# Kernel tuning notes

Measured on AMD Instinct MI355X. Metric: run time of the kernel, lower is better.

## Reference

```python
import jax, jax.numpy as jnp
import numpy as np
from jax import lax

B, C, H, W, K = 32, 128, 56, 56, 5
CR = C // 4          # reduced channels in weight-gen MLP
CE = 4 * C           # expanded channels
EPS = 1e-6


def setup_inputs() -> dict:
    key = jax.random.key(0)
    ks = jax.random.split(key, 8)
    s = lambda fan: 1.0 / np.sqrt(fan)
    return {
        "x": jax.random.normal(ks[0], (B, C, H, W), jnp.float32),
        "w_fc1": jax.random.normal(ks[1], (CR, C), jnp.float32) * s(C),
        "ln1_w": jnp.ones((CR,), jnp.float32),
        "ln1_b": jnp.zeros((CR,), jnp.float32),
        "w_fc2": jax.random.normal(ks[2], (C * K * K, CR), jnp.float32) * s(CR),
        "ln2_w": jnp.ones((C,), jnp.float32),
        "ln2_b": jnp.zeros((C,), jnp.float32),
        "w_expand": jax.random.normal(ks[3], (CE, C), jnp.float32) * s(C),
        "w_shrink": jax.random.normal(ks[4], (C, CE), jnp.float32) * s(CE),
        "grn_gamma": jax.random.normal(ks[5], (CE,), jnp.float32) * 0.1,
        "grn_beta": jax.random.normal(ks[6], (CE,), jnp.float32) * 0.1,
    }


def _ln(v, w, b, axis):
    u = v.mean(axis, keepdims=True)
    s2 = jnp.square(v - u).mean(axis, keepdims=True)
    return (v - u) * lax.rsqrt(s2 + EPS) * w + b


def reference(x, w_fc1, ln1_w, ln1_b, w_fc2, ln2_w, ln2_b, w_expand, w_shrink,
              grn_gamma, grn_beta):
    b, c, h, w = x.shape
    # ---- dynamic weight generation: pool -> fc1 -> LN -> fc2 ----
    pooled = x.mean((2, 3))                                  # [B, C]
    hdn = pooled @ w_fc1.T                                   # [B, CR]
    hdn = _ln(hdn, ln1_w, ln1_b, axis=-1)                    # channels_first LN over CR
    dyn = hdn @ w_fc2.T                                      # [B, C*K*K]
    dyn_w = dyn.reshape(b * c, 1, K, K)                      # per-sample depthwise kernels
    # ---- per-sample dynamic depthwise conv (groups = B*C) ----
    pad = K // 2
    out = lax.conv_general_dilated(
        x.reshape(1, b * c, h, w), dyn_w,
        window_strides=(1, 1), padding=[(pad, pad), (pad, pad)],
        dimension_numbers=("NCHW", "OIHW", "NCHW"),
        feature_group_count=b * c,
    ).reshape(b, c, h, w)
    # ---- LN (channels_first) over channel dim ----
    u = out.mean(1, keepdims=True)
    s2 = jnp.square(out - u).mean(1, keepdims=True)
    out = (out - u) * lax.rsqrt(s2 + EPS)
    out = ln2_w[None, :, None, None] * out + ln2_b[None, :, None, None]
    # ---- expand 1x1 -> GELU -> GRN -> shrink 1x1 ----
    out = jnp.einsum("bchw,oc->bohw", out, w_expand)         # [B, 4C, H, W]
    out = jax.nn.gelu(out, approximate=False)
    gx = jnp.sqrt(jnp.sum(jnp.square(out), axis=(2, 3), keepdims=True))  # [B,4C,1,1]
    nx = gx / (gx.mean(1, keepdims=True) + EPS)
    g = grn_gamma[None, :, None, None]
    bt = grn_beta[None, :, None, None]
    out = g * (out * nx) + bt + out
    out = jnp.einsum("bohw,co->bchw", out, w_shrink)         # [B, C, H, W]
    return out + x
```

## Files before the change

kernel.cpp:

```cpp
#include <hip/hip_runtime.h>
#include <hip/hip_bf16.h>

#define B_   32
#define C_   128
#define H_   56
#define W_   56
#define HW_  (H_*W_)
#define BHW_ (B_*HW_)
#define K5_  5
#define KK_  25
#define CR_  32
#define CE_  512
#define EPS_ 1e-6f

typedef __hip_bfloat16 bf16;
typedef __attribute__((ext_vector_type(8))) short short8;
typedef __attribute__((ext_vector_type(4))) float f32x4;


__device__ __forceinline__ float wave_reduce_sum(float v) {
#pragma unroll
  for (int off = 32; off > 0; off >>= 1) v += __shfl_down(v, off, 64);
  return v;
}
__device__ __forceinline__ float bf2f(unsigned short u) {
  return __uint_as_float(((unsigned)u) << 16);
}
__device__ __forceinline__ unsigned short f2bf_bits(float f) {
  bf16 h = __float2bfloat16(f);
  unsigned short u;
  __builtin_memcpy(&u, &h, 2);
  return u;
}
__device__ __forceinline__ float fast_gelu(float v) {
  float t = __expf(-1.702f * v);
  return v * __builtin_amdgcn_rcpf(1.0f + t);
}

__global__ __launch_bounds__(256) void prep_kernel(const float* __restrict__ we,
                                                   const float* __restrict__ ws,
                                                   bf16* __restrict__ weB,
                                                   bf16* __restrict__ wsB,
                                                   float* __restrict__ gx2) {
  int i = blockIdx.x * 256 + threadIdx.x;
  if (i < CE_ * C_)          weB[i] = __float2bfloat16(we[i]);
  else if (i < 2 * CE_ * C_) wsB[i - CE_ * C_] = __float2bfloat16(ws[i - CE_ * C_]);
  else                       gx2[i - 2 * CE_ * C_] = 0.f;
}

__global__ __launch_bounds__(256) void pool_kernel(const float* __restrict__ x,
                                                   float* __restrict__ pooled) {
  int bc = blockIdx.x;
  const float4* xp4 = reinterpret_cast<const float4*>(x + (size_t)bc * HW_);
  float s = 0.f;
  for (int i = threadIdx.x; i < 784; i += 256) {
    float4 v = xp4[i];
    s += (v.x + v.y) + (v.z + v.w);
  }
  s = wave_reduce_sum(s);
  __shared__ float red[4];
  int lane = threadIdx.x & 63, wid = threadIdx.x >> 6;
  if (lane == 0) red[wid] = s;
  __syncthreads();
  if (threadIdx.x == 0) pooled[bc] = (red[0] + red[1] + red[2] + red[3]) * (1.0f / HW_);
}

__global__ __launch_bounds__(256) void fc_kernel(const float* __restrict__ pooled,
                                                 const float* __restrict__ w_fc1,
                                                 const float* __restrict__ ln1_w,
                                                 const float* __restrict__ ln1_b,
                                                 const float* __restrict__ w_fc2,
                                                 float* __restrict__ dyn) {
  int b = blockIdx.x;
  int tid = threadIdx.x;
  __shared__ float sp[C_];
  __shared__ float sh[CR_];
  __shared__ float shn[CR_];
  __shared__ float stats[2];
  if (tid < C_) sp[tid] = pooled[b * C_ + tid];
  __syncthreads();
  if (tid < CR_) {
    float acc = 0.f;
    const float* wr = w_fc1 + tid * C_;
#pragma unroll 4
    for (int c = 0; c < C_; ++c) acc += sp[c] * wr[c];
    sh[tid] = acc;
  }
  __syncthreads();
  if (tid == 0) {
    float u = 0.f;
    for (int j = 0; j < CR_; ++j) u += sh[j];
    u *= (1.0f / CR_);
    float v = 0.f;
    for (int j = 0; j < CR_; ++j) { float d = sh[j] - u; v += d * d; }
    v *= (1.0f / CR_);
    stats[0] = u;
    stats[1] = rsqrtf(v + EPS_);
  }
  __syncthreads();
  if (tid < CR_) shn[tid] = (sh[tid] - stats[0]) * stats[1] * ln1_w[tid] + ln1_b[tid];
  __syncthreads();
  for (int i = tid; i < C_ * KK_; i += 256) {
    const float* wr = w_fc2 + i * CR_;
    float acc = 0.f;
#pragma unroll
    for (int j = 0; j < CR_; ++j) acc += shn[j] * wr[j];
    dyn[b * (C_ * KK_) + i] = acc;
  }
}

__global__ __launch_bounds__(256) void conv_kernel(const float* __restrict__ x,
                                                   const float* __restrict__ dyn,
                                                   bf16* __restrict__ z) {
  int bc = blockIdx.x;
  int b = bc >> 7;
  int c = bc & 127;
  int tid = threadIdx.x;
  __shared__ float xs[(H_ + 4) * 64];
  __shared__ float wks[KK_];
  {
    int r = tid >> 6;
    int rr = (r < 2) ? r : (56 + r);
    xs[rr * 64 + (tid & 63)] = 0.f;
  }
  if (tid < 224) {
    int r = tid >> 2, q = tid & 3;
    int col = (q < 2) ? q : (56 + q);
    xs[(r + 2) * 64 + col] = 0.f;
  }
  if (tid < KK_) wks[tid] = dyn[b * (C_ * KK_) + c * KK_ + tid];
  const float4* xp4 = reinterpret_cast<const float4*>(x + (size_t)bc * HW_);
  for (int i = tid; i < 784; i += 256) {
    float4 v = xp4[i];
    int h = i / 14, w4 = (i % 14) * 4;
    float* dst = &xs[(h + 2) * 64 + 2 + w4];
    dst[0] = v.x; dst[1] = v.y; dst[2] = v.z; dst[3] = v.w;
  }
  __syncthreads();
  float wr[KK_];
#pragma unroll
  for (int j = 0; j < KK_; ++j) wr[j] = wks[j];
  for (int g = tid; g < 784; g += 256) {
    int h = g / 14;
    int w4 = (g % 14) * 4;
    float a0 = 0.f, a1 = 0.f, a2 = 0.f, a3 = 0.f;
#pragma unroll
    for (int dh = 0; dh < K5_; ++dh) {
      const float* row = &xs[(h + dh) * 64 + w4];
      float4 va = *reinterpret_cast<const float4*>(row);
      float4 vb = *reinterpret_cast<const float4*>(row + 4);
      float v0 = va.x, v1 = va.y, v2 = va.z, v3 = va.w;
      float v4 = vb.x, v5 = vb.y, v6 = vb.z, v7 = vb.w;
      float u0 = wr[dh * 5 + 0], u1 = wr[dh * 5 + 1], u2 = wr[dh * 5 + 2];
      float u3 = wr[dh * 5 + 3], u4 = wr[dh * 5 + 4];
      a0 += v0 * u0 + v1 * u1 + v2 * u2 + v3 * u3 + v4 * u4;
      a1 += v1 * u0 + v2 * u1 + v3 * u2 + v4 * u3 + v5 * u4;
      a2 += v2 * u0 + v3 * u1 + v4 * u2 + v5 * u3 + v6 * u4;
      a3 += v3 * u0 + v4 * u1 + v5 * u2 + v6 * u3 + v7 * u4;
    }
    size_t base = (size_t)bc * HW_ + h * W_ + w4;
    ushort4 pk = make_ushort4(f2bf_bits(a0), f2bf_bits(a1), f2bf_bits(a2), f2bf_bits(a3));
    *reinterpret_cast<ushort4*>(reinterpret_cast<unsigned short*>(z) + base) = pk;
  }
}

__global__ __launch_bounds__(256) void ln_kernel(const bf16* __restrict__ z,
                                                 const float* __restrict__ ln2_w,
                                                 const float* __restrict__ ln2_b,
                                                 bf16* __restrict__ yT) {
  int hw0 = blockIdx.x * 64;
  int b = blockIdx.y;
  int tid = threadIdx.x;
  int wq = tid & 63;
  int cq = tid >> 6;
  __shared__ unsigned short zt[C_][64];
  __shared__ unsigned short yt[64][136];
  __shared__ float redS[4][64];
  __shared__ float redQ[4][64];
  __shared__ float meanArr[64];
  __shared__ float invArr[64];
  float s = 0.f, q = 0.f;
  const unsigned short* zp = reinterpret_cast<const unsigned short*>(z);
#pragma unroll 4
  for (int k = 0; k < 32; ++k) {
    int c = cq * 32 + k;
    unsigned short u = zp[((size_t)(b * C_ + c)) * HW_ + hw0 + wq];
    float v = bf2f(u);
    s += v;
    q += v * v;
    zt[c][wq] = u;
  }
  redS[cq][wq] = s;
  redQ[cq][wq] = q;
  __syncthreads();
  if (cq == 0) {
    float ss = redS[0][wq] + redS[1][wq] + redS[2][wq] + redS[3][wq];
    float qq = redQ[0][wq] + redQ[1][wq] + redQ[2][wq] + redQ[3][wq];
    float m = ss * (1.0f / C_);
    float var = qq * (1.0f / C_) - m * m;
    meanArr[wq] = m;
    invArr[wq] = rsqrtf(fmaxf(var, 0.f) + EPS_);
  }
  __syncthreads();
  float m = meanArr[wq], iv = invArr[wq];
#pragma unroll
  for (int g = 0; g < 4; ++g) {
    unsigned short pk[8];
#pragma unroll
    for (int i = 0; i < 8; ++i) {
      int c = cq * 32 + g * 8 + i;
      float v = bf2f(zt[c][wq]);
      pk[i] = f2bf_bits((v - m) * iv * ln2_w[c] + ln2_b[c]);
    }
    int4 t;
    __builtin_memcpy(&t, pk, 16);
    *reinterpret_cast<int4*>(&yt[wq][cq * 32 + g * 8]) = t;
  }
  __syncthreads();
  unsigned short* yp = reinterpret_cast<unsigned short*>(yT);
#pragma unroll
  for (int i = 0; i < 4; ++i) {
    int t = tid + 256 * i;
    int row = t >> 4, ch = t & 15;
    int4 v = *reinterpret_cast<const int4*>(&yt[row][ch * 8]);
    *reinterpret_cast<int4*>(yp + ((size_t)(b * HW_ + hw0 + row)) * C_ + ch * 8) = v;
  }
}

__global__ __launch_bounds__(256, 4) void expand_mfma(const bf16* __restrict__ yT,
                                                      const bf16* __restrict__ weB,
                                                      bf16* __restrict__ eT,
                                                      float* __restrict__ gx2) {
  int o0 = blockIdx.x * 128;
  int j0 = blockIdx.y * 128;
  int tid = threadIdx.x;
  int lane = tid & 63, wid = tid >> 6;
  int wm = wid >> 1, wn = wid & 1;
  int quad = lane >> 4, l15 = lane & 15;
  __shared__ __align__(16) char smem[128 * 136 * 2];
  short (*As)[40] = reinterpret_cast<short(*)[40]>(&smem[0]);
  short (*Bs)[40] = reinterpret_cast<short(*)[40]>(&smem[10240]);
  f32x4 acc[4][4] = {};
  const short* yTs = reinterpret_cast<const short*>(yT);
  const short* weS = reinterpret_cast<const short*>(weB);
  for (int k0 = 0; k0 < C_; k0 += 32) {
#pragma unroll
    for (int t = tid; t < 512; t += 256) {
      int r = t >> 2, ch = t & 3;
      int4 va = *reinterpret_cast<const int4*>(yTs + (size_t)(j0 + r) * C_ + k0 + ch * 8);
      *reinterpret_cast<int4*>(&As[r][ch * 8]) = va;
      int4 vb = *reinterpret_cast<const int4*>(weS + (size_t)(o0 + r) * C_ + k0 + ch * 8);
      *reinterpret_cast<int4*>(&Bs[r][ch * 8]) = vb;
    }
    __syncthreads();
    short8 a[4], bfr[4];
#pragma unroll
    for (int mf = 0; mf < 4; ++mf)
      a[mf] = *reinterpret_cast<const short8*>(&As[wm * 64 + mf * 16 + l15][quad * 8]);
#pragma unroll
    for (int nf = 0; nf < 4; ++nf)
      bfr[nf] = *reinterpret_cast<const short8*>(&Bs[wn * 64 + nf * 16 + l15][quad * 8]);
#pragma unroll
    for (int mf = 0; mf < 4; ++mf)
#pragma unroll
      for (int nf = 0; nf < 4; ++nf)
        acc[mf][nf] = __builtin_amdgcn_mfma_f32_16x16x32_bf16(a[mf], bfr[nf], acc[mf][nf], 0, 0, 0);
    __syncthreads();
  }
  short (*Es)[136] = reinterpret_cast<short(*)[136]>(&smem[0]);
#pragma unroll
  for (int mf = 0; mf < 4; ++mf) {
    int jm = j0 + wm * 64 + mf * 16;
    int bb = jm / HW_;
    int jrow = wm * 64 + mf * 16 + quad * 4;
#pragma unroll
    for (int nf = 0; nf < 4; ++nf) {
      int oc = wn * 64 + nf * 16 + l15;
      float g2 = 0.f;
#pragma unroll
      for (int r = 0; r < 4; ++r) {
        float ge = fast_gelu(acc[mf][nf][r]);
        g2 += ge * ge;
        Es[jrow + r][oc] = (short)f2bf_bits(ge);
      }
      g2 += __shfl_xor(g2, 16, 64);
      g2 += __shfl_xor(g2, 32, 64);
      if (quad == 0) atomicAdd(&gx2[bb * CE_ + o0 + oc], g2);
    }
  }
  __syncthreads();
  unsigned short* eP = reinterpret_cast<unsigned short*>(eT);
#pragma unroll
  for (int i = 0; i < 8; ++i) {
    int t = tid + 256 * i;
    int row = t >> 4, ch = t & 15;
    int4 v = *reinterpret_cast<const int4*>(&Es[row][ch * 8]);
    *reinterpret_cast<int4*>(eP + (size_t)(j0 + row) * CE_ + o0 + ch * 8) = v;
  }
}

__global__ __launch_bounds__(512) void grn_scale_kernel(const float* __restrict__ gx2,
                                                        const float* __restrict__ gamma,
                                                        float* __restrict__ scale) {
  int b = blockIdx.x;
  int o = threadIdx.x;
  float gx = sqrtf(gx2[b * CE_ + o]);
  float s = wave_reduce_sum(gx);
  __shared__ float red[8];
  __shared__ float meansh;
  int lane = o & 63, wid = o >> 6;
  if (lane == 0) red[wid] = s;
  __syncthreads();
  if (o == 0) {
    float t = 0.f;
    for (int i = 0; i < 8; ++i) t += red[i];
    meansh = t * (1.0f / CE_);
  }
  __syncthreads();
  scale[b * CE_ + o] = 1.0f + gamma[o] * (gx / (meansh + EPS_));
}

__global__ __launch_bounds__(256) void sb_kernel(const float* __restrict__ w_shrink,
                                                 const float* __restrict__ beta,
                                                 float* __restrict__ sb) {
  int c = blockIdx.x;
  const float* wp = w_shrink + (size_t)c * CE_;
  float acc = 0.f;
  for (int o = threadIdx.x; o < CE_; o += 256) acc += wp[o] * beta[o];
  acc = wave_reduce_sum(acc);
  __shared__ float red[4];
  int lane = threadIdx.x & 63, wid = threadIdx.x >> 6;
  if (lane == 0) red[wid] = acc;
  __syncthreads();
  if (threadIdx.x == 0) sb[c] = red[0] + red[1] + red[2] + red[3];
}

__global__ __launch_bounds__(256, 4) void shrink_mfma(const bf16* __restrict__ eT,
                                                      const bf16* __restrict__ wsB,
                                                      const float* __restrict__ scale,
                                                      const float* __restrict__ sb,
                                                      const float* __restrict__ x,
                                                      float* __restrict__ out) {
  int hw0 = blockIdx.x * 128;
  int b = blockIdx.y;
  int tid = threadIdx.x;
  int lane = tid & 63, wid = tid >> 6;
  int wm = wid >> 1, wn = wid & 1;
  int quad = lane >> 4, l15 = lane & 15;
  __shared__ __align__(16) char smem[36864];
  short (*As)[72] = reinterpret_cast<short(*)[72]>(&smem[0]);
  short (*Bs)[72] = reinterpret_cast<short(*)[72]>(&smem[18432]);
  const short* eS  = reinterpret_cast<const short*>(eT) + (size_t)b * HW_ * CE_;
  const short* wsS = reinterpret_cast<const short*>(wsB);
  const float* scp = scale + b * CE_;
  f32x4 acc[4][4] = {};
#pragma unroll 1
  for (int kc = 0; kc < 8; ++kc) {
    int k0 = kc * 64;
#pragma unroll
    for (int i = 0; i < 4; ++i) {
      int t = tid + 256 * i;
      int row = t >> 3, ch = t & 7;
      int hwc = hw0 + row; if (hwc >= HW_) hwc = HW_ - 1;
      *reinterpret_cast<int4*>(&As[row][ch * 8]) =
          *reinterpret_cast<const int4*>(eS + (size_t)hwc * CE_ + k0 + ch * 8);
      int4 wv = *reinterpret_cast<const int4*>(wsS + (size_t)row * CE_ + k0 + ch * 8);
      float4 s0 = *reinterpret_cast<const float4*>(scp + k0 + ch * 8);
      float4 s1 = *reinterpret_cast<const float4*>(scp + k0 + ch * 8 + 4);
      unsigned short wu[8];
      __builtin_memcpy(wu, &wv, 16);
      unsigned short ru[8];
      ru[0] = f2bf_bits(bf2f(wu[0]) * s0.x);
      ru[1] = f2bf_bits(bf2f(wu[1]) * s0.y);
      ru[2] = f2bf_bits(bf2f(wu[2]) * s0.z);
      ru[3] = f2bf_bits(bf2f(wu[3]) * s0.w);
      ru[4] = f2bf_bits(bf2f(wu[4]) * s1.x);
      ru[5] = f2bf_bits(bf2f(wu[5]) * s1.y);
      ru[6] = f2bf_bits(bf2f(wu[6]) * s1.z);
      ru[7] = f2bf_bits(bf2f(wu[7]) * s1.w);
      int4 rv;
      __builtin_memcpy(&rv, ru, 16);
      *reinterpret_cast<int4*>(&Bs[row][ch * 8]) = rv;
    }
    __syncthreads();
#pragma unroll
    for (int ks = 0; ks < 2; ++ks) {
      short8 a[4], bfr[4];
#pragma unroll
      for (int mf = 0; mf < 4; ++mf)
        a[mf] = *reinterpret_cast<const short8*>(&As[wm * 64 + mf * 16 + l15][ks * 32 + quad * 8]);
#pragma unroll
      for (int nf = 0; nf < 4; ++nf)
        bfr[nf] = *reinterpret_cast<const short8*>(&Bs[wn * 64 + nf * 16 + l15][ks * 32 + quad * 8]);
#pragma unroll
      for (int mf = 0; mf < 4; ++mf)
#pragma unroll
        for (int nf = 0; nf < 4; ++nf)
          acc[mf][nf] = __builtin_amdgcn_mfma_f32_16x16x32_bf16(a[mf], bfr[nf], acc[mf][nf], 0, 0, 0);
    }
    __syncthreads();
  }
  float (*Ef)[132] = reinterpret_cast<float(*)[132]>(&smem[0]);
#pragma unroll 1
  for (int phase = 0; phase < 2; ++phase) {
    if (wn == phase) {
#pragma unroll
      for (int mf = 0; mf < 4; ++mf) {
        int hwr = wm * 64 + mf * 16 + quad * 4;
#pragma unroll
        for (int nf = 0; nf < 4; ++nf)
          *reinterpret_cast<f32x4*>(&Ef[nf * 16 + l15][hwr]) = acc[mf][nf];
      }
    }
    __syncthreads();
#pragma unroll
    for (int i = 0; i < 8; ++i) {
      int t = tid + 256 * i;
      int row = t >> 5, ch = t & 31;
      int hw = hw0 + ch * 4;
      if (hw < HW_) {
        int c = phase * 64 + row;
        size_t base = ((size_t)(b * C_ + c)) * HW_ + hw;
        float add = sb[c];
        f32x4 av = *reinterpret_cast<const f32x4*>(&Ef[row][ch * 4]);
        float4 xv = *reinterpret_cast<const float4*>(x + base);
        float4 ov;
        ov.x = av.x + add + xv.x;
        ov.y = av.y + add + xv.y;
        ov.z = av.z + add + xv.z;
        ov.w = av.w + add + xv.w;
        *reinterpret_cast<float4*>(out + base) = ov;
      }
    }
    __syncthreads();
  }
}

extern "C" void kernel_launch(void* const* d_in, const int* in_sizes, int n_in,
                              void* d_out, int out_size, void* d_ws, size_t ws_size,
                              hipStream_t stream) {
  (void)in_sizes; (void)n_in; (void)out_size; (void)ws_size;
  const float* x        = (const float*)d_in[0];
  const float* w_fc1    = (const float*)d_in[1];
  const float* ln1_w    = (const float*)d_in[2];
  const float* ln1_b    = (const float*)d_in[3];
  const float* w_fc2    = (const float*)d_in[4];
  const float* ln2_w    = (const float*)d_in[5];
  const float* ln2_b    = (const float*)d_in[6];
  const float* w_expand = (const float*)d_in[7];
  const float* w_shrink = (const float*)d_in[8];
  const float* gamma    = (const float*)d_in[9];
  const float* beta     = (const float*)d_in[10];
  float* out = (float*)d_out;

  char* ws = (char*)d_ws;
  float* pooled = (float*)(ws + 0);
  float* dyn    = (float*)(ws + 16384);
  float* gx2    = (float*)(ws + 425984);
  float* scale  = (float*)(ws + 491520);
  float* sb     = (float*)(ws + 557056);
  bf16*  weB    = (bf16*)(ws + 557568);
  bf16*  wsB    = (bf16*)(ws + 688640);
  bf16*  yT     = (bf16*)(ws + 819712);
  bf16*  eT     = (bf16*)(ws + 26509824);
  bf16*  z      = eT;

  prep_kernel<<<576, 256, 0, stream>>>(w_expand, w_shrink, weB, wsB, gx2);
  sb_kernel<<<C_, 256, 0, stream>>>(w_shrink, beta, sb);
  pool_kernel<<<B_ * C_, 256, 0, stream>>>(x, pooled);
  fc_kernel<<<B_, 256, 0, stream>>>(pooled, w_fc1, ln1_w, ln1_b, w_fc2, dyn);
  conv_kernel<<<B_ * C_, 256, 0, stream>>>(x, dyn, z);
  ln_kernel<<<dim3(49, B_), 256, 0, stream>>>(z, ln2_w, ln2_b, yT);
  expand_mfma<<<dim3(4, 784), 256, 0, stream>>>(yT, weB, eT, gx2);
  grn_scale_kernel<<<B_, 512, 0, stream>>>(gx2, gamma, scale);
  shrink_mfma<<<dim3(25, B_), 256, 0, stream>>>(eT, wsB, scale, sb, x, out);
}
```

Measured before the change: 271.0 us.

## Double-buffer GEMM staging with direct global-to-LDS loads and XOR swizzle

Both MFMA GEMMs now stage tiles with global_load_lds directly into double-buffered, XOR-swizzled shared memory, so the next k-tile's load overlaps the current compute and bank conflicts are avoided. The per-batch GRN scale is folded into the shrink weights once by a new scale_ws_kernel, which removes the per-tile scaling arithmetic from the shrink GEMM. The expand grid order is swapped, and shrink occupancy drops to 2 blocks because it now uses 64KB of LDS. The scaled weights reuse the yT workspace region, which is safe only because yT is dead after expand.

```diff
diff --git a/kernel.cpp b/kernel.cpp
--- a/kernel.cpp
+++ b/kernel.cpp
@@ -35,6 +35,11 @@
 __device__ __forceinline__ float fast_gelu(float v) {
   float t = __expf(-1.702f * v);
   return v * __builtin_amdgcn_rcpf(1.0f + t);
+}
+__device__ __forceinline__ void glds16(const void* g, void* l) {
+  __builtin_amdgcn_global_load_lds(
+      (const __attribute__((address_space(1))) unsigned int*)g,
+      (__attribute__((address_space(3))) unsigned int*)l, 16, 0, 0);
 }
 
 __global__ __launch_bounds__(256) void prep_kernel(const float* __restrict__ we,
@@ -231,35 +236,43 @@
                                                       const bf16* __restrict__ weB,
                                                       bf16* __restrict__ eT,
                                                       float* __restrict__ gx2) {
-  int o0 = blockIdx.x * 128;
-  int j0 = blockIdx.y * 128;
+  int j0 = blockIdx.x * 128;
+  int o0 = blockIdx.y * 128;
   int tid = threadIdx.x;
   int lane = tid & 63, wid = tid >> 6;
   int wm = wid >> 1, wn = wid & 1;
   int quad = lane >> 4, l15 = lane & 15;
-  __shared__ __align__(16) char smem[128 * 136 * 2];
-  short (*As)[40] = reinterpret_cast<short(*)[40]>(&smem[0]);
-  short (*Bs)[40] = reinterpret_cast<short(*)[40]>(&smem[10240]);
+  __shared__ __align__(16) char smem[34816];
+  const short* yS = reinterpret_cast<const short*>(yT);
+  const short* weS = reinterpret_cast<const short*>(weB);
+  int sr = (wid * 2) * 16 + (lane >> 2);
+  int scp = lane & 3;
+  auto STAGE = [&](int bs, int k0) {
+#pragma unroll
+    for (int i = 0; i < 2; ++i) {
+      int seg = wid * 2 + i;
+      int r = sr + i * 16;
+      int c = scp ^ ((r >> 1) & 3);
+      char* base = smem + bs * 16384 + seg * 1024;
+      glds16(yS + (size_t)(j0 + r) * C_ + k0 + c * 8, base);
+      glds16(weS + (size_t)(o0 + r) * C_ + k0 + c * 8, base + 8192);
+    }
+  };
   f32x4 acc[4][4] = {};
-  const short* yTs = reinterpret_cast<const short*>(yT);
-  const short* weS = reinterpret_cast<const short*>(weB);
-  for (int k0 = 0; k0 < C_; k0 += 32) {
-#pragma unroll
-    for (int t = tid; t < 512; t += 256) {
-      int r = t >> 2, ch = t & 3;
-      int4 va = *reinterpret_cast<const int4*>(yTs + (size_t)(j0 + r) * C_ + k0 + ch * 8);
-      *reinterpret_cast<int4*>(&As[r][ch * 8]) = va;
-      int4 vb = *reinterpret_cast<const int4*>(weS + (size_t)(o0 + r) * C_ + k0 + ch * 8);
-      *reinterpret_cast<int4*>(&Bs[r][ch * 8]) = vb;
-    }
-    __syncthreads();
+  STAGE(0, 0);
+  __syncthreads();
+#pragma unroll
+  for (int t = 0; t < 4; ++t) {
+    if (t < 3) STAGE((t + 1) & 1, (t + 1) * 32);
+    const char* ba = smem + (t & 1) * 16384;
+    int sx = (quad ^ ((l15 >> 1) & 3)) * 16;
     short8 a[4], bfr[4];
 #pragma unroll
     for (int mf = 0; mf < 4; ++mf)
-      a[mf] = *reinterpret_cast<const short8*>(&As[wm * 64 + mf * 16 + l15][quad * 8]);
+      a[mf] = *reinterpret_cast<const short8*>(ba + (wm * 64 + mf * 16 + l15) * 64 + sx);
 #pragma unroll
     for (int nf = 0; nf < 4; ++nf)
-      bfr[nf] = *reinterpret_cast<const short8*>(&Bs[wn * 64 + nf * 16 + l15][quad * 8]);
+      bfr[nf] = *reinterpret_cast<const short8*>(ba + 8192 + (wn * 64 + nf * 16 + l15) * 64 + sx);
 #pragma unroll
     for (int mf = 0; mf < 4; ++mf)
 #pragma unroll
@@ -335,9 +348,20 @@
   if (threadIdx.x == 0) sb[c] = red[0] + red[1] + red[2] + red[3];
 }
 
-__global__ __launch_bounds__(256, 4) void shrink_mfma(const bf16* __restrict__ eT,
-                                                      const bf16* __restrict__ wsB,
-                                                      const float* __restrict__ scale,
+__global__ __launch_bounds__(256) void scale_ws_kernel(const float* __restrict__ ws,
+                                                       const float* __restrict__ scale,
+                                                       bf16* __restrict__ sws) {
+  int c = blockIdx.x;
+  int b = blockIdx.y;
+  const float* sp = scale + b * CE_;
+  const float* wp = ws + (size_t)c * CE_;
+  bf16* op = sws + ((size_t)(b * C_ + c)) * CE_;
+  for (int i = threadIdx.x; i < CE_; i += 256)
+    op[i] = __float2bfloat16(wp[i] * sp[i]);
+}
+
+__global__ __launch_bounds__(256, 2) void shrink_mfma(const bf16* __restrict__ eT,
+                                                      const bf16* __restrict__ sws,
                                                       const float* __restrict__ sb,
                                                       const float* __restrict__ x,
                                                       float* __restrict__ out) {
@@ -347,51 +371,43 @@
   int lane = tid & 63, wid = tid >> 6;
   int wm = wid >> 1, wn = wid & 1;
   int quad = lane >> 4, l15 = lane & 15;
-  __shared__ __align__(16) char smem[36864];
-  short (*As)[72] = reinterpret_cast<short(*)[72]>(&smem[0]);
-  short (*Bs)[72] = reinterpret_cast<short(*)[72]>(&smem[18432]);
+  __shared__ __align__(16) char smem[65536];
   const short* eS  = reinterpret_cast<const short*>(eT) + (size_t)b * HW_ * CE_;
-  const short* wsS = reinterpret_cast<const short*>(wsB);
-  const float* scp = scale + b * CE_;
+  const short* wsS = reinterpret_cast<const short*>(sws) + (size_t)b * C_ * CE_;
+  int sr0 = (wid * 4) * 8 + (lane >> 3);
+  int scp = lane & 7;
+  auto STAGE = [&](int bs, int k0) {
+#pragma unroll
+    for (int i = 0; i < 4; ++i) {
+      int seg = wid * 4 + i;
+      int r = sr0 + i * 8;
+      int c = scp ^ (r & 7);
+      int hwc = hw0 + r; if (hwc >= HW_) hwc = HW_ - 1;
+      char* base = smem + bs * 32768 + seg * 1024;
+      glds16(eS + (size_t)hwc * CE_ + k0 + c * 8, base);
+      glds16(wsS + (size_t)r * CE_ + k0 + c * 8, base + 16384);
+    }
+  };
   f32x4 acc[4][4] = {};
+  STAGE(0, 0);
+  __syncthreads();
 #pragma unroll 1
-  for (int kc = 0; kc < 8; ++kc) {
-    int k0 = kc * 64;
-#pragma unroll
-    for (int i = 0; i < 4; ++i) {
-      int t = tid + 256 * i;
-      int row = t >> 3, ch = t & 7;
-      int hwc = hw0 + row; if (hwc >= HW_) hwc = HW_ - 1;
-      *reinterpret_cast<int4*>(&As[row][ch * 8]) =
-          *reinterpret_cast<const int4*>(eS + (size_t)hwc * CE_ + k0 + ch * 8);
-      int4 wv = *reinterpret_cast<const int4*>(wsS + (size_t)row * CE_ + k0 + ch * 8);
-      float4 s0 = *reinterpret_cast<const float4*>(scp + k0 + ch * 8);
-      float4 s1 = *reinterpret_cast<const float4*>(scp + k0 + ch * 8 + 4);
-      unsigned short wu[8];
-      __builtin_memcpy(wu, &wv, 16);
-      unsigned short ru[8];
-      ru[0] = f2bf_bits(bf2f(wu[0]) * s0.x);
-      ru[1] = f2bf_bits(bf2f(wu[1]) * s0.y);
-      ru[2] = f2bf_bits(bf2f(wu[2]) * s0.z);
-      ru[3] = f2bf_bits(bf2f(wu[3]) * s0.w);
-      ru[4] = f2bf_bits(bf2f(wu[4]) * s1.x);
-      ru[5] = f2bf_bits(bf2f(wu[5]) * s1.y);
-      ru[6] = f2bf_bits(bf2f(wu[6]) * s1.z);
-      ru[7] = f2bf_bits(bf2f(wu[7]) * s1.w);
-      int4 rv;
-      __builtin_memcpy(&rv, ru, 16);
-      *reinterpret_cast<int4*>(&Bs[row][ch * 8]) = rv;
-    }
-    __syncthreads();
+  for (int t = 0; t < 8; ++t) {
+    if (t < 7) STAGE((t + 1) & 1, (t + 1) * 64);
+    const char* ba = smem + (t & 1) * 32768;
 #pragma unroll
     for (int ks = 0; ks < 2; ++ks) {
       short8 a[4], bfr[4];
 #pragma unroll
-      for (int mf = 0; mf < 4; ++mf)
-        a[mf] = *reinterpret_cast<const short8*>(&As[wm * 64 + mf * 16 + l15][ks * 32 + quad * 8]);
-#pragma unroll
-      for (int nf = 0; nf < 4; ++nf)
-        bfr[nf] = *reinterpret_cast<const short8*>(&Bs[wn * 64 + nf * 16 + l15][ks * 32 + quad * 8]);
+      for (int mf = 0; mf < 4; ++mf) {
+        int cp = (ks * 4 + quad) ^ (l15 & 7);
+        a[mf] = *reinterpret_cast<const short8*>(ba + (wm * 64 + mf * 16 + l15) * 128 + cp * 16);
+      }
+#pragma unroll
+      for (int nf = 0; nf < 4; ++nf) {
+        int cp = (ks * 4 + quad) ^ (l15 & 7);
+        bfr[nf] = *reinterpret_cast<const short8*>(ba + 16384 + (wn * 64 + nf * 16 + l15) * 128 + cp * 16);
+      }
 #pragma unroll
       for (int mf = 0; mf < 4; ++mf)
 #pragma unroll
@@ -462,6 +478,7 @@
   bf16*  weB    = (bf16*)(ws + 557568);
   bf16*  wsB    = (bf16*)(ws + 688640);
   bf16*  yT     = (bf16*)(ws + 819712);
+  bf16*  sws    = (bf16*)(ws + 819712);
   bf16*  eT     = (bf16*)(ws + 26509824);
   bf16*  z      = eT;
 
@@ -471,7 +488,8 @@
   fc_kernel<<<B_, 256, 0, stream>>>(pooled, w_fc1, ln1_w, ln1_b, w_fc2, dyn);
   conv_kernel<<<B_ * C_, 256, 0, stream>>>(x, dyn, z);
   ln_kernel<<<dim3(49, B_), 256, 0, stream>>>(z, ln2_w, ln2_b, yT);
-  expand_mfma<<<dim3(4, 784), 256, 0, stream>>>(yT, weB, eT, gx2);
+  expand_mfma<<<dim3(784, 4), 256, 0, stream>>>(yT, weB, eT, gx2);
   grn_scale_kernel<<<B_, 512, 0, stream>>>(gx2, gamma, scale);
-  shrink_mfma<<<dim3(25, B_), 256, 0, stream>>>(eT, wsB, scale, sb, x, out);
-}
+  scale_ws_kernel<<<dim3(C_, B_), 256, 0, stream>>>(w_shrink, scale, sws);
+  shrink_mfma<<<dim3(25, B_), 256, 0, stream>>>(eT, sws, sb, x, out);
+}
```

After: 266.6 us. Within noise of the previous version (-1.6%).
